# Kernel tuning notes

Measured on AMD Instinct MI355X. Metric: run time of the kernel, lower is better.

## Reference

```python
import jax, jax.numpy as jnp
import numpy as np
from jax import lax

V, D, H, HD, L, E, HID, TOPK, B, T = 32000, 1024, 16, 64, 2, 4, 2048, 2, 1, 1024
EPS = 1e-8


def setup_inputs() -> dict:
    key = jax.random.key(0)
    ks = jax.random.split(key, 10)
    s = 0.02
    so = 0.02 / np.sqrt(2 * L)  # o_proj / down_proj init std
    return dict(
        idx=jax.random.randint(ks[0], (B, T), 0, V),
        tok_emb=jax.random.normal(ks[1], (V, D), jnp.float32) * s,
        attn_norm_w=jnp.ones((L, D), jnp.float32),
        q_w=jax.random.normal(ks[2], (L, D, D), jnp.float32) * s,
        q_b=jnp.zeros((L, D), jnp.float32),
        kv_w=jax.random.normal(ks[3], (L, D, 2 * D), jnp.float32) * s,
        kv_b=jnp.zeros((L, 2 * D), jnp.float32),
        o_w=jax.random.normal(ks[4], (L, D, D), jnp.float32) * so,
        o_b=jnp.zeros((L, D), jnp.float32),
        ffn_norm_w=jnp.ones((L, D), jnp.float32),
        router_w=jax.random.normal(ks[5], (L, D, E), jnp.float32) * s,
        gate_w=jax.random.normal(ks[6], (L, E, D, HID), jnp.float32) * s,
        up_w=jax.random.normal(ks[7], (L, E, D, HID), jnp.float32) * s,
        down_w=jax.random.normal(ks[8], (L, E, HID, D), jnp.float32) * so,
        lnf_w=jnp.ones((D,), jnp.float32),
    )


def _rms(x, w):
    return x / jnp.sqrt(jnp.mean(x * x, axis=-1, keepdims=True) + EPS) * w


def reference(idx, tok_emb, attn_norm_w, q_w, q_b, kv_w, kv_b, o_w, o_b,
              ffn_norm_w, router_w, gate_w, up_w, down_w, lnf_w):
    x = tok_emb[idx]  # [B,T,D]

    # ALiBi bias and causal mask (built once; block_size == T here)
    slopes = jnp.arange(1, H + 1, dtype=jnp.float32) / H          # [H]
    pos = jnp.arange(T, dtype=jnp.float32)
    alibi = slopes[:, None, None] * (pos[None, None, :] - pos[None, :, None])  # [H,T,T]
    causal = jnp.arange(T)[None, :] > jnp.arange(T)[:, None]      # True above diagonal

    for l in range(L):
        # --- causal self-attention with ALiBi ---
        h = _rms(x, attn_norm_w[l])
        q = (h @ q_w[l] + q_b[l]).reshape(B, T, H, HD)
        kv = (h @ kv_w[l] + kv_b[l]).reshape(B, T, 2, H, HD)
        k, v = kv[:, :, 0], kv[:, :, 1]
        att = jnp.einsum('bqhd,bkhd->bhqk', q, k) * (1.0 / np.sqrt(HD))
        att = att + alibi[None]
        att = jnp.where(causal, -jnp.inf, att)
        a = jax.nn.softmax(att, axis=-1)
        y = jnp.einsum('bhqk,bkhd->bqhd', a, v).reshape(B, T, D)
        x = x + y @ o_w[l] + o_b[l]

        # --- MoE FFN (top-k routing, SwiGLU experts, depth-scaled down_proj) ---
        hm = _rms(x, ffn_norm_w[l]).reshape(B * T, D)             # [N,D]
        rlog = hm @ router_w[l]                                   # [N,E]
        vals, sel = lax.top_k(rlog, TOPK)                         # [N,K]
        w = jax.nn.softmax(vals.astype(jnp.float32), axis=-1).astype(hm.dtype)
        # dense per-expert compute, combined sparsely via routing weights
        g = jax.nn.silu(jnp.einsum('nd,edh->enh', hm, gate_w[l])) \
            * jnp.einsum('nd,edh->enh', hm, up_w[l])              # [E,N,HID]
        out_e = jnp.einsum('enh,ehd->end', g, down_w[l]) * (1.0 / np.sqrt(l + 1))
        combine = jnp.sum(jax.nn.one_hot(sel, E, dtype=hm.dtype) * w[..., None], axis=1)  # [N,E]
        moe = jnp.einsum('ne,end->nd', combine, out_e).reshape(B, T, D)
        x = x + moe

    logits = _rms(x, lnf_w) @ tok_emb.T  # tied head weight
    return logits
```

## Files before the change

kernel.cpp:

```cpp
#include <hip/hip_runtime.h>
#include <cmath>

typedef __attribute__((ext_vector_type(8))) _Float16 f16x8;
typedef __attribute__((ext_vector_type(8))) unsigned short u16x8;
typedef __attribute__((ext_vector_type(4))) float f32x4;

#define DEV static __device__ __forceinline__

constexpr int Dm   = 1024;
constexpr int HIDm = 2048;
constexpr int NT   = 1024;
constexpr int NV   = 32000;
constexpr float EPSf  = 1e-8f;
constexpr float LOSC  = 4096.0f;
constexpr float ILOSC = 1.0f / 4096.0f;

DEV unsigned short h2u(_Float16 h){ union{_Float16 h; unsigned short u;} v; v.h=h; return v.u; }

DEV f32x4 MF(f16x8 a, f16x8 b, f32x4 c){ return __builtin_amdgcn_mfma_f32_16x16x32_f16(a,b,c,0,0,0); }

typedef __attribute__((address_space(1))) void GV;
typedef __attribute__((address_space(3))) void LV;
DEV void gll16(const void* g, void* l){
  __builtin_amdgcn_global_load_lds((GV*)(__UINTPTR_TYPE__)g, (LV*)l, 16, 0, 0);
}

DEV int swk(int lane){ return (((lane&3) ^ ((lane>>3)&3))*8); }
DEV int rdc(int fr, int fg){ return ((fg ^ ((fr>>1)&3))*8); }

template<int SPLIT>
DEV void st_sp(unsigned short* __restrict__ hi, unsigned short* __restrict__ lo, size_t o, float v){
  _Float16 hh = (_Float16)v;
  hi[o] = h2u(hh);
  if constexpr (SPLIT==3) lo[o] = h2u((_Float16)((v - (float)hh)*LOSC));
}

__global__ __launch_bounds__(256) void k_init(
    const int* __restrict__ idx, const float* __restrict__ emb,
    float* __restrict__ x, unsigned short* __restrict__ emb16, int gbase)
{
  const int b = blockIdx.x;
  if (b < gbase){
    const size_t i = ((size_t)b*256 + threadIdx.x)*8;
    const float4 v0 = *(const float4*)&emb[i];
    const float4 v1 = *(const float4*)&emb[i+4];
    u16x8 h;
    h[0]=h2u((_Float16)v0.x); h[1]=h2u((_Float16)v0.y);
    h[2]=h2u((_Float16)v0.z); h[3]=h2u((_Float16)v0.w);
    h[4]=h2u((_Float16)v1.x); h[5]=h2u((_Float16)v1.y);
    h[6]=h2u((_Float16)v1.z); h[7]=h2u((_Float16)v1.w);
    *(u16x8*)&emb16[i] = h;
  } else {
    const int t = b - gbase;
    const int d = threadIdx.x*4;
    *(float4*)&x[(size_t)t*Dm + d] = *(const float4*)&emb[(size_t)idx[t]*Dm + d];
  }
}

template<int SPLIT>
__global__ __launch_bounds__(256) void k_rms(
    const float* __restrict__ x, const float* __restrict__ w,
    unsigned short* __restrict__ ohi, unsigned short* __restrict__ olo)
{
  const int t = blockIdx.x, tid = threadIdx.x;
  const float* row = x + (size_t)t*Dm;
  float s = 0.f;
  #pragma unroll
  for (int i=0;i<4;++i){ const float v = row[tid + i*256]; s += v*v; }
  #pragma unroll
  for (int d=1; d<64; d<<=1) s += __shfl_xor(s, d);
  __shared__ float red[4];
  if ((tid&63)==0) red[tid>>6] = s;
  __syncthreads();
  const float tot = red[0]+red[1]+red[2]+red[3];
  const float rstd = rsqrtf(tot*(1.0f/Dm) + EPSf);
  #pragma unroll
  for (int i=0;i<4;++i){
    const int c = tid + i*256;
    st_sp<SPLIT>(ohi, olo, (size_t)t*Dm + c, row[c]*rstd*w[c]);
  }
}

template<int SPLIT>
__global__ __launch_bounds__(256) void k_fuse_o(
    const float* __restrict__ part, const float* __restrict__ ob,
    const float* __restrict__ fnw, const float* __restrict__ rw,
    float* __restrict__ x, unsigned short* __restrict__ hhi,
    unsigned short* __restrict__ hlo, float* __restrict__ cmb)
{
  const int t = blockIdx.x, tid = threadIdx.x, wv = tid>>6, lane = tid&63;
  const int c = tid*4;
  float4 s = *(float4*)&x[(size_t)t*Dm + c];
  #pragma unroll
  for (int z=0; z<4; ++z){
    const float4 p = *(const float4*)&part[((size_t)z*NT + t)*Dm + c];
    s.x+=p.x; s.y+=p.y; s.z+=p.z; s.w+=p.w;
  }
  const float4 b4 = *(const float4*)&ob[c];
  s.x+=b4.x; s.y+=b4.y; s.z+=b4.z; s.w+=b4.w;
  *(float4*)&x[(size_t)t*Dm + c] = s;

  float ss = s.x*s.x + s.y*s.y + s.z*s.z + s.w*s.w;
  #pragma unroll
  for (int d=1; d<64; d<<=1) ss += __shfl_xor(ss, d);
  __shared__ float red[4];
  if (lane==0) red[wv] = ss;
  __syncthreads();
  const float rstd = rsqrtf((red[0]+red[1]+red[2]+red[3])*(1.0f/Dm) + EPSf);

  const float4 w4 = *(const float4*)&fnw[c];
  const float sv[4] = {s.x,s.y,s.z,s.w};
  const float wv4[4] = {w4.x,w4.y,w4.z,w4.w};
  float hm[4];
  float lg[4] = {0.f,0.f,0.f,0.f};
  #pragma unroll
  for (int j=0;j<4;++j){
    hm[j] = sv[j]*rstd*wv4[j];
    st_sp<SPLIT>(hhi, hlo, (size_t)t*Dm + c + j, hm[j]);
    const float4 r4 = *(const float4*)&rw[(size_t)(c+j)*4];
    lg[0] += hm[j]*r4.x; lg[1] += hm[j]*r4.y; lg[2] += hm[j]*r4.z; lg[3] += hm[j]*r4.w;
  }
  #pragma unroll
  for (int d=1; d<64; d<<=1){
    lg[0]+=__shfl_xor(lg[0],d); lg[1]+=__shfl_xor(lg[1],d);
    lg[2]+=__shfl_xor(lg[2],d); lg[3]+=__shfl_xor(lg[3],d);
  }
  __shared__ float red2[4][4];
  if (lane==0){ red2[wv][0]=lg[0]; red2[wv][1]=lg[1]; red2[wv][2]=lg[2]; red2[wv][3]=lg[3]; }
  __syncthreads();
  if (tid==0){
    float L[4];
    #pragma unroll
    for (int e=0;e<4;++e) L[e] = red2[0][e]+red2[1][e]+red2[2][e]+red2[3][e];
    int s0 = 0;
    for (int e=1;e<4;++e) if (L[e] > L[s0]) s0 = e;
    int s1 = -1;
    for (int e=0;e<4;++e){ if (e==s0) continue; if (s1<0 || L[e] > L[s1]) s1 = e; }
    const float eb2 = expf(L[s1] - L[s0]);
    const float inv = 1.0f/(1.0f + eb2);
    float o[4] = {0.f,0.f,0.f,0.f};
    o[s0] = inv; o[s1] = eb2*inv;
    cmb[t*4+0]=o[0]; cmb[t*4+1]=o[1]; cmb[t*4+2]=o[2]; cmb[t*4+3]=o[3];
  }
}

__global__ __launch_bounds__(256) void k_fuse_moe(
    const float* __restrict__ part, const float* __restrict__ cmb,
    const float* __restrict__ w, float* __restrict__ x,
    unsigned short* __restrict__ dst, int writex)
{
  const int t = blockIdx.x, tid = threadIdx.x, wv = tid>>6, lane = tid&63;
  const int c = tid*4;
  float4 s = *(float4*)&x[(size_t)t*Dm + c];
  #pragma unroll
  for (int e=0; e<4; ++e){
    if (cmb[(size_t)t*4 + e] > 0.f){
      const float4 p0 = *(const float4*)&part[((size_t)(e*2+0)*NT + t)*Dm + c];
      const float4 p1 = *(const float4*)&part[((size_t)(e*2+1)*NT + t)*Dm + c];
      s.x+=p0.x+p1.x; s.y+=p0.y+p1.y; s.z+=p0.z+p1.z; s.w+=p0.w+p1.w;
    }
  }
  if (writex) *(float4*)&x[(size_t)t*Dm + c] = s;
  float ss = s.x*s.x + s.y*s.y + s.z*s.z + s.w*s.w;
  #pragma unroll
  for (int d=1; d<64; d<<=1) ss += __shfl_xor(ss, d);
  __shared__ float red[4];
  if (lane==0) red[wv] = ss;
  __syncthreads();
  const float rstd = rsqrtf((red[0]+red[1]+red[2]+red[3])*(1.0f/Dm) + EPSf);
  const float4 w4 = *(const float4*)&w[c];
  const float sv[4] = {s.x,s.y,s.z,s.w};
  const float wv4[4] = {w4.x,w4.y,w4.z,w4.w};
  #pragma unroll
  for (int j=0;j<4;++j)
    dst[(size_t)t*Dm + c + j] = h2u((_Float16)(sv[j]*rstd*wv4[j]));
}

__global__ __launch_bounds__(256) void k_scan(
    const float* __restrict__ cmb, int* __restrict__ tl,
    float* __restrict__ cwl, int* __restrict__ cnt)
{
  const int e = threadIdx.x>>6, lane = threadIdx.x&63;
  int base = 0;
  for (int t0=0; t0<NT; t0+=64){
    const float w = cmb[(size_t)(t0+lane)*4 + e];
    const unsigned long long m = __ballot(w > 0.f);
    const int pre = __popcll(m & ((1ull<<lane)-1ull));
    if (w > 0.f){ tl[e*NT + base + pre] = t0+lane; cwl[e*NT + base + pre] = w; }
    base += __popcll(m);
  }
  if (lane==0) cnt[e] = base;
}

template<int SPLIT>
DEV void wconv_tile(const float* __restrict__ W, unsigned short* __restrict__ Whi,
                    unsigned short* __restrict__ Wlo, int K, int N, int n0, int k0,
                    float (*tile)[65], int t)
{
  const int r = t>>2;
  #pragma unroll
  for (int i=0;i<4;++i){
    const int c = (t&3)*16 + i*4;
    *(float4*)&tile[r][c] = *(const float4*)&W[(size_t)(k0+r)*N + n0 + c];
  }
  __syncthreads();
  const int n = t>>2;
  #pragma unroll
  for (int i=0;i<2;++i){
    const int kc = (t&3)*8 + i*32;
    u16x8 hi, lo;
    #pragma unroll
    for (int j=0;j<8;++j){
      const float v = tile[kc+j][n];
      const _Float16 hh = (_Float16)v;
      hi[j] = h2u(hh);
      if constexpr (SPLIT==3) lo[j] = h2u((_Float16)((v-(float)hh)*LOSC));
      else lo[j] = 0;
    }
    *(u16x8*)&Whi[(size_t)(n0+n)*K + k0 + kc] = hi;
    if constexpr (SPLIT==3) *(u16x8*)&Wlo[(size_t)(n0+n)*K + k0 + kc] = lo;
  }
}

template<int SPLIT>
__global__ __launch_bounds__(256) void k_wconv(
    const float* __restrict__ W, unsigned short* __restrict__ Whi,
    unsigned short* __restrict__ Wlo, int K, int N)
{
  __shared__ float tile[64][65];
  const size_t eb = (size_t)blockIdx.z * (size_t)K * N;
  wconv_tile<SPLIT>(W + eb, Whi + eb, Wlo + eb, K, N, blockIdx.x*64, blockIdx.y*64,
                    tile, threadIdx.x);
}

template<int SPLIT>
__global__ __launch_bounds__(256) void k_wconv_qkvo(
    const float* __restrict__ qw, const float* __restrict__ kvw, const float* __restrict__ ow,
    unsigned short* __restrict__ Wh, unsigned short* __restrict__ Wl,
    unsigned short* __restrict__ WOh, unsigned short* __restrict__ WOl)
{
  __shared__ float tile[64][65];
  const int b = blockIdx.x, t = threadIdx.x;
  if (b < 256){
    wconv_tile<SPLIT>(qw, Wh, Wl, Dm, Dm, (b&15)*64, (b>>4)*64, tile, t);
  } else if (b < 768){
    const int c = b - 256;
    wconv_tile<SPLIT>(kvw, Wh + (size_t)Dm*Dm, Wl + (size_t)Dm*Dm,
                      Dm, 2*Dm, (c&31)*64, (c>>5)*64, tile, t);
  } else {
    const int c = b - 768;
    wconv_tile<SPLIT>(ow, WOh, WOl, Dm, Dm, (c&15)*64, (c>>4)*64, tile, t);
  }
}

template<int SPLIT>
__global__ __launch_bounds__(256) void k_wconv_gu(
    const float* __restrict__ gw, const float* __restrict__ uw,
    unsigned short* __restrict__ WGh, unsigned short* __restrict__ WGl,
    unsigned short* __restrict__ WUh, unsigned short* __restrict__ WUl)
{
  __shared__ float tile[64][65];
  const int b = blockIdx.x, t = threadIdx.x;
  const int half = b >> 11;
  const int c = b & 2047;
  const int e = c >> 9, cc = c & 511;
  const size_t eb = (size_t)e * (size_t)Dm * HIDm;
  const int n0 = (cc&31)*64, k0 = (cc>>5)*64;
  if (half == 0)
    wconv_tile<SPLIT>(gw + eb, WGh + eb, WGl + eb, Dm, HIDm, n0, k0, tile, t);
  else
    wconv_tile<SPLIT>(uw + eb, WUh + eb, WUl + eb, Dm, HIDm, n0, k0, tile, t);
}

template<int SPLIT, int ZMODE>
__global__ __launch_bounds__(256) void k_mm(
    const unsigned short* __restrict__ Ahi, const unsigned short* __restrict__ Alo,
    const unsigned short* __restrict__ Bhi, const unsigned short* __restrict__ Blo,
    float* __restrict__ part, int lda, int ldb, int K, int ldo, int nx)
{
  constexpr int PL = (SPLIT==3)?2:1;
  __shared__ __align__(16) unsigned short As[PL][128][32];
  __shared__ __align__(16) unsigned short Bs[PL][128][32];
  const int xcd = blockIdx.x & 7, ii = blockIdx.x >> 3;
  const int w = xcd * (int)(gridDim.x >> 3) + ii;
  const int g = w >> 3, yy = w & 7;
  const int n0 = (g % nx)*128, r0 = yy*128, zz = g / nx;
  const int tid=threadIdx.x, wv=tid>>6, lane=tid&63, fr=lane&15, fg=lane>>4;
  const int wr=(wv>>1)*64, wc=(wv&1)*64;
  const int sr=lane>>2, sk=swk(lane);
  const int rc = rdc(fr, fg);

  const f32x4 z4={0.f,0.f,0.f,0.f};
  f32x4 accM[4][4], accC[4][4];
  #pragma unroll
  for (int i=0;i<4;++i)
    #pragma unroll
    for (int j=0;j<4;++j){ accM[i][j]=z4; accC[i][j]=z4; }

  for (int kt=0; kt<K; kt+=32){
    #pragma unroll
    for (int i=0;i<2;++i){
      const int rr = wv*32 + i*16 + sr;
      size_t ao, bo;
      if constexpr (ZMODE==2){
        ao = (size_t)(r0+rr)*lda + zz*K + kt + sk;
        bo = (size_t)(n0+rr)*ldb + zz*K + kt + sk;
      } else {
        ao = (size_t)(r0+rr)*lda + kt + sk;
        bo = (size_t)(n0+rr)*ldb + kt + sk;
      }
      gll16(&Ahi[ao], &As[0][wv*32+i*16][0]);
      if constexpr (SPLIT==3) gll16(&Alo[ao], &As[1][wv*32+i*16][0]);
      gll16(&Bhi[bo], &Bs[0][wv*32+i*16][0]);
      if constexpr (SPLIT==3) gll16(&Blo[bo], &Bs[1][wv*32+i*16][0]);
    }
    __syncthreads();
    f16x8 a[4][PL], b[4][PL];
    #pragma unroll
    for (int rt=0;rt<4;++rt)
      #pragma unroll
      for (int p=0;p<PL;++p) a[rt][p] = *(const f16x8*)&As[p][wr+rt*16+fr][rc];
    #pragma unroll
    for (int ct=0;ct<4;++ct)
      #pragma unroll
      for (int p=0;p<PL;++p) b[ct][p] = *(const f16x8*)&Bs[p][wc+ct*16+fr][rc];
    #pragma unroll
    for (int rt=0;rt<4;++rt)
      #pragma unroll
      for (int ct=0;ct<4;++ct){
        accM[rt][ct] = MF(a[rt][0], b[ct][0], accM[rt][ct]);
        if constexpr (SPLIT==3){
          accC[rt][ct] = MF(a[rt][0], b[ct][1], accC[rt][ct]);
          accC[rt][ct] = MF(a[rt][1], b[ct][0], accC[rt][ct]);
        }
      }
    __syncthreads();
  }

  #pragma unroll
  for (int rt=0;rt<4;++rt)
    #pragma unroll
    for (int ct=0;ct<4;++ct)
      #pragma unroll
      for (int j=0;j<4;++j){
        const int row = r0 + wr + rt*16 + fg*4 + j;
        const int col = n0 + wc + ct*16 + fr;
        float v = accM[rt][ct][j];
        if constexpr (SPLIT==3) v += accC[rt][ct][j]*ILOSC;
        part[((size_t)zz*NT + row)*ldo + col] = v;
      }
}

template<int SPLIT>
__global__ __launch_bounds__(256) void k_comb_qkvt(
    const float* __restrict__ part, const float* __restrict__ qb, const float* __restrict__ kvb,
    unsigned short* __restrict__ qhi, unsigned short* __restrict__ qlo,
    unsigned short* __restrict__ khi, unsigned short* __restrict__ klo,
    unsigned short* __restrict__ vthi, unsigned short* __restrict__ vtlo)
{
  __shared__ float tile[64][65];
  const int bid = blockIdx.x, tid = threadIdx.x;
  if (bid < 1024){
    const int t = bid;
    #pragma unroll
    for (int i=0;i<2;++i){
      const int col = tid*4 + i*1024;
      const float4 p0 = *(const float4*)&part[(size_t)t*3072 + col];
      const float4 p1 = *(const float4*)&part[((size_t)NT + t)*3072 + col];
      float v[4] = {p0.x+p1.x, p0.y+p1.y, p0.z+p1.z, p0.w+p1.w};
      #pragma unroll
      for (int j=0;j<4;++j){
        const int c = col + j;
        if (c < Dm) st_sp<SPLIT>(qhi, qlo, (size_t)t*Dm + c, v[j] + qb[c]);
        else        st_sp<SPLIT>(khi, klo, (size_t)t*Dm + (c-Dm), v[j] + kvb[c-Dm]);
      }
    }
  } else {
    const int c = bid - 1024;
    const int d0 = (c&15)*64, t0 = (c>>4)*64;
    {
      const int tl_ = tid>>2, dc = (tid&3)*16;
      #pragma unroll
      for (int i=0;i<4;++i){
        const int d = dc + i*4;
        const float4 p0 = *(const float4*)&part[(size_t)(t0+tl_)*3072 + 2048 + d0 + d];
        const float4 p1 = *(const float4*)&part[((size_t)NT + t0+tl_)*3072 + 2048 + d0 + d];
        tile[tl_][d+0] = p0.x+p1.x + kvb[1024+d0+d+0];
        tile[tl_][d+1] = p0.y+p1.y + kvb[1024+d0+d+1];
        tile[tl_][d+2] = p0.z+p1.z + kvb[1024+d0+d+2];
        tile[tl_][d+3] = p0.w+p1.w + kvb[1024+d0+d+3];
      }
    }
    __syncthreads();
    #pragma unroll
    for (int i=0;i<2;++i){
      const int u = tid + i*256;
      const int dl = u>>3, tch = (u&7)*8;
      u16x8 hi, lo;
      #pragma unroll
      for (int j=0;j<8;++j){
        const float v = tile[tch+j][dl];
        const _Float16 hh = (_Float16)v;
        hi[j] = h2u(hh);
        if constexpr (SPLIT==3) lo[j] = h2u((_Float16)((v-(float)hh)*LOSC));
        else lo[j] = 0;
      }
      *(u16x8*)&vthi[(size_t)(d0+dl)*NT + t0 + tch] = hi;
      if constexpr (SPLIT==3) *(u16x8*)&vtlo[(size_t)(d0+dl)*NT + t0 + tch] = lo;
    }
  }
}

template<int SPLIT>
__global__ __launch_bounds__(256) void k_down(
    const unsigned short* __restrict__ Ahi, const unsigned short* __restrict__ Alo,
    const unsigned short* __restrict__ Bhi, const unsigned short* __restrict__ Blo,
    const int* __restrict__ tl, const int* __restrict__ cnt,
    float* __restrict__ part)
{
  constexpr int PL = (SPLIT==3)?2:1;
  const int xcd = blockIdx.x & 7, ii = blockIdx.x >> 3;
  const int w = xcd*64 + ii;
  const int g = w >> 3, yy = w & 7;
  const int zz = g >> 3, e = zz >> 1, ks = zz & 1;
  const int r0 = yy*128, n0 = (g&7)*128;
  const int cn = cnt[e];
  if (r0 >= cn) return;
  __shared__ __align__(16) unsigned short As[PL][128][32];
  __shared__ __align__(16) unsigned short Bs[PL][128][32];
  __shared__ int tl_s[128];
  const int tid=threadIdx.x, wv=tid>>6, lane=tid&63, fr=lane&15, fg=lane>>4;
  const int wr=(wv>>1)*64, wc=(wv&1)*64;
  const int sr=lane>>2, sk=swk(lane);
  const int rc = rdc(fr, fg);
  if (tid < 128) tl_s[tid] = (r0+tid < cn) ? tl[e*NT + r0 + tid] : -1;

  const f32x4 z4={0.f,0.f,0.f,0.f};
  f32x4 accM[4][4], accC[4][4];
  #pragma unroll
  for (int i=0;i<4;++i)
    #pragma unroll
    for (int j=0;j<4;++j){ accM[i][j]=z4; accC[i][j]=z4; }

  const int kbeg = ks*1024, kend = kbeg + 1024;
  for (int kt=kbeg; kt<kend; kt+=32){
    #pragma unroll
    for (int i=0;i<2;++i){
      const int rr = wv*32 + i*16 + sr;
      const size_t ao = (size_t)((e<<10) + r0 + rr)*HIDm + kt + sk;
      const size_t bo = (size_t)e*((size_t)Dm*HIDm) + (size_t)(n0+rr)*HIDm + kt + sk;
      gll16(&Ahi[ao], &As[0][wv*32+i*16][0]);
      if constexpr (SPLIT==3) gll16(&Alo[ao], &As[1][wv*32+i*16][0]);
      gll16(&Bhi[bo], &Bs[0][wv*32+i*16][0]);
      if constexpr (SPLIT==3) gll16(&Blo[bo], &Bs[1][wv*32+i*16][0]);
    }
    __syncthreads();
    f16x8 a[4][PL], b[4][PL];
    #pragma unroll
    for (int rt=0;rt<4;++rt)
      #pragma unroll
      for (int p=0;p<PL;++p) a[rt][p] = *(const f16x8*)&As[p][wr+rt*16+fr][rc];
    #pragma unroll
    for (int ct=0;ct<4;++ct)
      #pragma unroll
      for (int p=0;p<PL;++p) b[ct][p] = *(const f16x8*)&Bs[p][wc+ct*16+fr][rc];
    #pragma unroll
    for (int rt=0;rt<4;++rt)
      #pragma unroll
      for (int ct=0;ct<4;++ct){
        accM[rt][ct] = MF(a[rt][0], b[ct][0], accM[rt][ct]);
        if constexpr (SPLIT==3){
          accC[rt][ct] = MF(a[rt][0], b[ct][1], accC[rt][ct]);
          accC[rt][ct] = MF(a[rt][1], b[ct][0], accC[rt][ct]);
        }
      }
    __syncthreads();
  }

  #pragma unroll
  for (int rt=0;rt<4;++rt)
    #pragma unroll
    for (int ct=0;ct<4;++ct)
      #pragma unroll
      for (int j=0;j<4;++j){
        const int i = wr + rt*16 + fg*4 + j;
        const int col = n0 + wc + ct*16 + fr;
        float v = accM[rt][ct][j];
        if constexpr (SPLIT==3) v += accC[rt][ct][j]*ILOSC;
        const int tok = tl_s[i];
        if (tok >= 0) part[((size_t)zz*NT + tok)*Dm + col] = v;
      }
}

template<int SPLIT>
__global__ __launch_bounds__(512) void k_guf(
    const unsigned short* __restrict__ Ahi, const unsigned short* __restrict__ Alo,
    const unsigned short* __restrict__ Ghi, const unsigned short* __restrict__ Glo,
    const unsigned short* __restrict__ Uhi, const unsigned short* __restrict__ Ulo,
    const int* __restrict__ tl, const float* __restrict__ cwl, const int* __restrict__ cnt,
    unsigned short* __restrict__ Hhi, unsigned short* __restrict__ Hlo, float scale)
{
  constexpr int PL=(SPLIT==3)?2:1;
  const int xcd = blockIdx.x & 7, ii = blockIdx.x >> 3;
  const int w = xcd*128 + ii;
  const int g = w >> 3, yy = w & 7;
  const int e = g >> 5, n0 = (g & 31)*64, r0 = yy*128;
  const int cn = cnt[e];
  if (r0 >= cn) return;
  __shared__ __align__(16) unsigned short As[PL][128][32];
  __shared__ __align__(16) unsigned short Gs[PL][64][32];
  __shared__ __align__(16) unsigned short Us[PL][64][32];
  __shared__ float cw_s[128];
  const int tid=threadIdx.x, wv=tid>>6, lane=tid&63, fr=lane&15, fg=lane>>4;
  const int wr=(wv>>1)*32, wc=(wv&1)*32;
  const int sr=lane>>2, sk=swk(lane);
  const int rc = rdc(fr, fg);
  const size_t ebW = (size_t)e * ((size_t)HIDm*Dm);
  if (tid < 128) cw_s[tid] = (r0+tid < cn) ? cwl[e*NT + r0 + tid]*scale : 0.f;

  const int lrA = r0 + wv*16 + sr;
  const int tokA = tl[e*NT + (lrA < cn ? lrA : cn-1)];
  const size_t abase = (size_t)tokA*Dm + sk;
  const int rrB = (wv&3)*16 + sr;
  const size_t bbase = ebW + (size_t)(n0+rrB)*Dm + sk;

  const f32x4 z4={0.f,0.f,0.f,0.f};
  f32x4 aGM[2][2],aGC[2][2],aUM[2][2],aUC[2][2];
  #pragma unroll
  for (int i=0;i<2;++i)
    #pragma unroll
    for (int j=0;j<2;++j){ aGM[i][j]=z4; aGC[i][j]=z4; aUM[i][j]=z4; aUC[i][j]=z4; }

  for (int kt=0; kt<Dm; kt+=32){
    gll16(&Ahi[abase + kt], &As[0][wv*16][0]);
    if constexpr (SPLIT==3) gll16(&Alo[abase + kt], &As[1][wv*16][0]);
    if (wv < 4){
      gll16(&Ghi[bbase + kt], &Gs[0][(wv&3)*16][0]);
      if constexpr (SPLIT==3) gll16(&Glo[bbase + kt], &Gs[1][(wv&3)*16][0]);
    } else {
      gll16(&Uhi[bbase + kt], &Us[0][(wv&3)*16][0]);
      if constexpr (SPLIT==3) gll16(&Ulo[bbase + kt], &Us[1][(wv&3)*16][0]);
    }
    __syncthreads();
    f16x8 a[2][PL], bg[2][PL], bu[2][PL];
    #pragma unroll
    for (int rt=0;rt<2;++rt)
      #pragma unroll
      for (int p=0;p<PL;++p) a[rt][p] = *(const f16x8*)&As[p][wr+rt*16+fr][rc];
    #pragma unroll
    for (int ct=0;ct<2;++ct)
      #pragma unroll
      for (int p=0;p<PL;++p){
        bg[ct][p] = *(const f16x8*)&Gs[p][wc+ct*16+fr][rc];
        bu[ct][p] = *(const f16x8*)&Us[p][wc+ct*16+fr][rc];
      }
    #pragma unroll
    for (int rt=0;rt<2;++rt)
      #pragma unroll
      for (int ct=0;ct<2;++ct){
        aGM[rt][ct] = MF(a[rt][0], bg[ct][0], aGM[rt][ct]);
        aUM[rt][ct] = MF(a[rt][0], bu[ct][0], aUM[rt][ct]);
        if constexpr (SPLIT==3){
          aGC[rt][ct] = MF(a[rt][0], bg[ct][1], aGC[rt][ct]);
          aGC[rt][ct] = MF(a[rt][1], bg[ct][0], aGC[rt][ct]);
          aUC[rt][ct] = MF(a[rt][0], bu[ct][1], aUC[rt][ct]);
          aUC[rt][ct] = MF(a[rt][1], bu[ct][0], aUC[rt][ct]);
        }
      }
    __syncthreads();
  }
  #pragma unroll
  for (int rt=0;rt<2;++rt)
    #pragma unroll
    for (int ct=0;ct<2;++ct)
      #pragma unroll
      for (int j=0;j<4;++j){
        const int i = wr + rt*16 + fg*4 + j;
        const int row = r0 + i;
        const int col = n0 + wc + ct*16 + fr;
        float g2 = aGM[rt][ct][j], u = aUM[rt][ct][j];
        if constexpr (SPLIT==3){ g2 += aGC[rt][ct][j]*ILOSC; u += aUC[rt][ct][j]*ILOSC; }
        const float cw = cw_s[i];
        const float h = (g2/(1.0f + expf(-g2))) * u * cw;
        st_sp<SPLIT>(Hhi, Hlo, (size_t)((e<<10) + row)*HIDm + col, h);
      }
}

__global__ __launch_bounds__(256) void k_lg(
    const unsigned short* __restrict__ Ahi, const float* __restrict__ emb,
    float* __restrict__ out)
{
  __shared__ __align__(16) unsigned short As[128][32];
  __shared__ __align__(16) unsigned short Bs[128][32];
  const int tid=threadIdx.x, wv=tid>>6, lane=tid&63, fr=lane&15, fg=lane>>4;
  const int w = (blockIdx.x & 7)*250 + (blockIdx.x >> 3);
  const int n0 = (w>>3)*128, r0 = (w&7)*128;
  const int wr=(wv>>1)*64, wc=(wv&1)*64;
  const int sr=lane>>2, sk=swk(lane);
  const int rc = rdc(fr, fg);
  const int br = tid>>1;
  const f32x4 z4={0.f,0.f,0.f,0.f};
  f32x4 acc[4][4];
  #pragma unroll
  for (int i=0;i<4;++i)
    #pragma unroll
    for (int j=0;j<4;++j) acc[i][j]=z4;

  for (int kt=0; kt<Dm; kt+=32){
    #pragma unroll
    for (int i=0;i<2;++i){
      const int rr = wv*32 + i*16 + sr;
      gll16(&Ahi[(size_t)(r0+rr)*Dm + kt + sk], &As[wv*32+i*16][0]);
    }
    {
      const int bc = (tid&1)*16;
      const float* s = &emb[(size_t)(n0+br)*Dm + kt + bc];
      const float4 v0 = *(const float4*)s;
      const float4 v1 = *(const float4*)(s+4);
      const float4 v2 = *(const float4*)(s+8);
      const float4 v3 = *(const float4*)(s+12);
      u16x8 h0, h1;
      h0[0]=h2u((_Float16)v0.x); h0[1]=h2u((_Float16)v0.y);
      h0[2]=h2u((_Float16)v0.z); h0[3]=h2u((_Float16)v0.w);
      h0[4]=h2u((_Float16)v1.x); h0[5]=h2u((_Float16)v1.y);
      h0[6]=h2u((_Float16)v1.z); h0[7]=h2u((_Float16)v1.w);
      h1[0]=h2u((_Float16)v2.x); h1[1]=h2u((_Float16)v2.y);
      h1[2]=h2u((_Float16)v2.z); h1[3]=h2u((_Float16)v2.w);
      h1[4]=h2u((_Float16)v3.x); h1[5]=h2u((_Float16)v3.y);
      h1[6]=h2u((_Float16)v3.z); h1[7]=h2u((_Float16)v3.w);
      const int s_ = (br>>1)&3;
      const int u0 = (tid&1)*2;
      *(u16x8*)&Bs[br][(u0^s_)*8]     = h0;
      *(u16x8*)&Bs[br][((u0+1)^s_)*8] = h1;
    }
    __syncthreads();
    f16x8 a[4], b[4];
    #pragma unroll
    for (int rt=0;rt<4;++rt) a[rt] = *(const f16x8*)&As[wr+rt*16+fr][rc];
    #pragma unroll
    for (int ct=0;ct<4;++ct) b[ct] = *(const f16x8*)&Bs[wc+ct*16+fr][rc];
    #pragma unroll
    for (int rt=0;rt<4;++rt)
      #pragma unroll
      for (int ct=0;ct<4;++ct) acc[rt][ct] = MF(a[rt], b[ct], acc[rt][ct]);
    __syncthreads();
  }
  #pragma unroll
  for (int rt=0;rt<4;++rt)
    #pragma unroll
    for (int ct=0;ct<4;++ct)
      #pragma unroll
      for (int j=0;j<4;++j)
        out[(size_t)(r0+wr+rt*16+fg*4+j)*NV + n0+wc+ct*16+fr] = acc[rt][ct][j];
}

__global__ __launch_bounds__(512) void k_lg16(
    const unsigned short* __restrict__ Ahi, const unsigned short* __restrict__ B16,
    float* __restrict__ out)
{
  __shared__ __align__(16) unsigned short As[256][64];
  __shared__ __align__(16) unsigned short Bs[256][64];
  const int tid=threadIdx.x, wv=tid>>6, lane=tid&63, fr=lane&15, fg=lane>>4;
  const int xcd = blockIdx.x & 7, ii = blockIdx.x >> 3;
  const int w = (xcd < 4 ? xcd*63 : 252 + (xcd-4)*62) + ii;
  const int n0 = (w>>2)*256, r0 = (w&3)*256;
  const int wrow=(wv>>2)*128, wcol=(wv&3)*64;
  const int srow = lane>>3;
  const int sk = (((lane&7) ^ srow)*8);
  const f32x4 z4={0.f,0.f,0.f,0.f};
  f32x4 acc[8][4];
  #pragma unroll
  for (int i=0;i<8;++i)
    #pragma unroll
    for (int j=0;j<4;++j) acc[i][j]=z4;

  for (int kt=0; kt<Dm; kt+=64){
    #pragma unroll
    for (int i=0;i<4;++i){
      const int rr = wv*32 + i*8 + srow;
      gll16(&Ahi[(size_t)(r0+rr)*Dm + kt + sk], &As[wv*32+i*8][0]);
      gll16(&B16[(size_t)(n0+rr)*Dm + kt + sk], &Bs[wv*32+i*8][0]);
    }
    __syncthreads();
    #pragma unroll
    for (int kk=0;kk<2;++kk){
      f16x8 a[8], b[4];
      #pragma unroll
      for (int rt=0;rt<8;++rt)
        a[rt] = *(const f16x8*)&As[wrow+rt*16+fr][(((kk*4+fg) ^ (fr&7))*8)];
      #pragma unroll
      for (int ct=0;ct<4;++ct)
        b[ct] = *(const f16x8*)&Bs[wcol+ct*16+fr][(((kk*4+fg) ^ (fr&7))*8)];
      #pragma unroll
      for (int rt=0;rt<8;++rt)
        #pragma unroll
        for (int ct=0;ct<4;++ct) acc[rt][ct] = MF(a[rt], b[ct], acc[rt][ct]);
    }
    __syncthreads();
  }
  #pragma unroll
  for (int rt=0;rt<8;++rt)
    #pragma unroll
    for (int ct=0;ct<4;++ct)
      #pragma unroll
      for (int j=0;j<4;++j)
        out[(size_t)(r0+wrow+rt*16+fg*4+j)*NV + n0+wcol+ct*16+fr] = acc[rt][ct][j];
}

template<int SPLIT>
__global__ __launch_bounds__(256) void k_attn(
    const unsigned short* __restrict__ qhi, const unsigned short* __restrict__ qlo,
    const unsigned short* __restrict__ khi, const unsigned short* __restrict__ klo,
    const unsigned short* __restrict__ vthi, const unsigned short* __restrict__ vtlo,
    unsigned short* __restrict__ yhi, unsigned short* __restrict__ ylo)
{
  constexpr int PL = (SPLIT==3) ? 2 : 1;
  const int qt = blockIdx.x, hd = blockIdx.y;
  const int tid = threadIdx.x, wv = tid>>6, lane = tid&63;
  const int fr = lane&15, fg = lane>>4;
  const int rbase = qt*64 + wv*16;
  const float slope = (float)(hd+1) * (1.0f/16.0f);

  __shared__ __align__(16) unsigned short Ps[4][PL][16][32];

  f16x8 aq[2][PL];
  #pragma unroll
  for (int c=0;c<2;++c){
    const size_t off = (size_t)(rbase+fr)*Dm + hd*64 + c*32 + fg*8;
    aq[c][0] = *(const f16x8*)&qhi[off];
    if constexpr (SPLIT==3) aq[c][1] = *(const f16x8*)&qlo[off];
  }

  const f32x4 z4 = {0.f,0.f,0.f,0.f};
  f32x4 yM[4], yC[4];
  #pragma unroll
  for (int ct=0;ct<4;++ct){ yM[ct]=z4; yC[ct]=z4; }
  float m[4], lsum[4];
  #pragma unroll
  for (int j=0;j<4;++j){ m[j] = -INFINITY; lsum[j] = 0.f; }

  const int nkt = qt*2 + 2;
  for (int kt=0; kt<nkt; ++kt){
    f32x4 sM[2], sC[2];
    sM[0]=z4; sM[1]=z4; sC[0]=z4; sC[1]=z4;
    #pragma unroll
    for (int kh=0; kh<2; ++kh){
      #pragma unroll
      for (int c=0;c<2;++c){
        const size_t off = (size_t)(kt*32 + kh*16 + fr)*Dm + hd*64 + c*32 + fg*8;
        const f16x8 b0 = *(const f16x8*)&khi[off];
        sM[kh] = MF(aq[c][0], b0, sM[kh]);
        if constexpr (SPLIT==3){
          const f16x8 b1 = *(const f16x8*)&klo[off];
          sC[kh] = MF(aq[c][0], b1, sC[kh]);
          sC[kh] = MF(aq[c][1], b0, sC[kh]);
        }
      }
    }
    float sv[2][4], mx[4];
    #pragma unroll
    for (int j=0;j<4;++j) mx[j] = -INFINITY;
    #pragma unroll
    for (int kh=0; kh<2; ++kh)
      #pragma unroll
      for (int j=0;j<4;++j){
        const int kcol = kt*32 + kh*16 + fr;
        const int row  = rbase + fg*4 + j;
        float s = sM[kh][j];
        if constexpr (SPLIT==3) s += sC[kh][j]*ILOSC;
        s = s*0.125f + slope*(float)(kcol - row);
        sv[kh][j] = (kcol > row) ? -INFINITY : s;
        mx[j] = fmaxf(mx[j], sv[kh][j]);
      }
    #pragma unroll
    for (int d=1; d<16; d<<=1)
      #pragma unroll
      for (int j=0;j<4;++j) mx[j] = fmaxf(mx[j], __shfl_xor(mx[j], d));
    float resc[4];
    #pragma unroll
    for (int j=0;j<4;++j){
      const float mn = fmaxf(m[j], mx[j]);
      resc[j] = expf(m[j] - mn);
      m[j] = mn;
    }
    float p[2][4], psum[4];
    #pragma unroll
    for (int j=0;j<4;++j) psum[j] = 0.f;
    #pragma unroll
    for (int kh=0;kh<2;++kh)
      #pragma unroll
      for (int j=0;j<4;++j){
        const float pv = (sv[kh][j] == -INFINITY) ? 0.f : expf(sv[kh][j] - m[j]);
        p[kh][j] = pv; psum[j] += pv;
      }
    #pragma unroll
    for (int d=1; d<16; d<<=1)
      #pragma unroll
      for (int j=0;j<4;++j) psum[j] += __shfl_xor(psum[j], d);
    #pragma unroll
    for (int j=0;j<4;++j) lsum[j] = lsum[j]*resc[j] + psum[j];
    #pragma unroll
    for (int ct=0;ct<4;++ct)
      #pragma unroll
      for (int j=0;j<4;++j){ yM[ct][j]*=resc[j]; yC[ct][j]*=resc[j]; }
    #pragma unroll
    for (int kh=0;kh<2;++kh)
      #pragma unroll
      for (int j=0;j<4;++j){
        const float pv = p[kh][j];
        _Float16 ph = (_Float16)pv;
        Ps[wv][0][fg*4+j][kh*16+fr] = h2u(ph);
        if constexpr (SPLIT==3)
          Ps[wv][1][fg*4+j][kh*16+fr] = h2u((_Float16)((pv-(float)ph)*LOSC));
      }
    asm volatile("s_waitcnt lgkmcnt(0)" ::: "memory");
    f16x8 pa[PL];
    pa[0] = *(const f16x8*)&Ps[wv][0][fr][fg*8];
    if constexpr (SPLIT==3) pa[1] = *(const f16x8*)&Ps[wv][1][fr][fg*8];
    #pragma unroll
    for (int ct=0;ct<4;++ct){
      const size_t off = (size_t)(hd*64 + ct*16 + fr)*NT + kt*32 + fg*8;
      const f16x8 v0 = *(const f16x8*)&vthi[off];
      yM[ct] = MF(pa[0], v0, yM[ct]);
      if constexpr (SPLIT==3){
        const f16x8 v1 = *(const f16x8*)&vtlo[off];
        yC[ct] = MF(pa[0], v1, yC[ct]);
        yC[ct] = MF(pa[1], v0, yC[ct]);
      }
    }
    asm volatile("s_waitcnt lgkmcnt(0)" ::: "memory");
  }
  #pragma unroll
  for (int ct=0;ct<4;++ct)
    #pragma unroll
    for (int j=0;j<4;++j){
      float v = yM[ct][j];
      if constexpr (SPLIT==3) v += yC[ct][j]*ILOSC;
      v /= lsum[j];
      const size_t off = (size_t)(rbase + fg*4 + j)*Dm + hd*64 + ct*16 + fr;
      st_sp<SPLIT>(yhi, ylo, off, v);
    }
}

struct Ptrs {
  float* x; float* cmb; float* part; float* cwl; int* tl; int* cnt;
  unsigned short *hhi,*hlo,*qhi,*qlo,*khi,*klo,*vthi,*vtlo,*yhi,*ylo,*Hhi,*Hlo;
  unsigned short *Wqkvh,*Wqkvl,*WOh,*WOl,*WGh,*WGl,*WUh,*WUl,*WDh,*WDl;
};

template<int S>
static void run_layer(const Ptrs& P, int l,
    const float* anw, const float* qw, const float* qb, const float* kvw, const float* kvb,
    const float* ow, const float* ob, const float* fnw, const float* rw,
    const float* gw, const float* uw, const float* dw,
    const float* nextw, unsigned short* nextdst, int writex, float scale, hipStream_t stream)
{
  (void)anw;
  k_wconv_qkvo<S><<<dim3(1024), dim3(256), 0, stream>>>(
      qw + (size_t)l*Dm*Dm, kvw + (size_t)l*Dm*2*Dm, ow + (size_t)l*Dm*Dm,
      P.Wqkvh, P.Wqkvl, P.WOh, P.WOl);
  k_mm<S,2><<<dim3(384), dim3(256), 0, stream>>>(P.hhi, P.hlo, P.Wqkvh, P.Wqkvl,
      P.part, Dm, Dm, 512, 3072, 24);
  k_comb_qkvt<S><<<dim3(1280), dim3(256), 0, stream>>>(P.part, qb + l*Dm, kvb + l*2*Dm,
      P.qhi, P.qlo, P.khi, P.klo, P.vthi, P.vtlo);
  k_attn<S><<<dim3(16,16), dim3(256), 0, stream>>>(P.qhi,P.qlo,P.khi,P.klo,P.vthi,P.vtlo,P.yhi,P.ylo);
  k_mm<S,2><<<dim3(256), dim3(256), 0, stream>>>(P.yhi, P.ylo, P.WOh, P.WOl,
      P.part, Dm, Dm, 256, Dm, 8);
  k_fuse_o<S><<<dim3(NT), dim3(256), 0, stream>>>(P.part, ob + l*Dm, fnw + l*Dm,
      rw + (size_t)l*Dm*4, P.x, P.hhi, P.hlo, P.cmb);
  k_scan<<<dim3(1), dim3(256), 0, stream>>>(P.cmb, P.tl, P.cwl, P.cnt);
  k_wconv_gu<S><<<dim3(4096), dim3(256), 0, stream>>>(
      gw + (size_t)l*4*Dm*HIDm, uw + (size_t)l*4*Dm*HIDm, P.WGh, P.WGl, P.WUh, P.WUl);
  k_guf<S><<<dim3(1024), dim3(512), 0, stream>>>(P.hhi, P.hlo, P.WGh, P.WGl, P.WUh, P.WUl,
      P.tl, P.cwl, P.cnt, P.Hhi, P.Hlo, scale);
  k_wconv<S><<<dim3(16,32,4), dim3(256), 0, stream>>>(dw + (size_t)l*4*HIDm*Dm, P.WDh, P.WDl, HIDm, Dm);
  k_down<S><<<dim3(512), dim3(256), 0, stream>>>(P.Hhi, P.Hlo, P.WDh, P.WDl,
      P.tl, P.cnt, P.part);
  k_fuse_moe<<<dim3(NT), dim3(256), 0, stream>>>(P.part, P.cmb, nextw, P.x, nextdst, writex);
}

extern "C" void kernel_launch(void* const* d_in, const int* in_sizes, int n_in,
                              void* d_out, int out_size, void* d_ws, size_t ws_size,
                              hipStream_t stream)
{
  (void)in_sizes; (void)n_in; (void)out_size;
  const int*   idx = (const int*)d_in[0];
  const float* emb = (const float*)d_in[1];
  const float* anw = (const float*)d_in[2];
  const float* qw  = (const float*)d_in[3];
  const float* qb  = (const float*)d_in[4];
  const float* kvw = (const float*)d_in[5];
  const float* kvb = (const float*)d_in[6];
  const float* ow  = (const float*)d_in[7];
  const float* ob  = (const float*)d_in[8];
  const float* fnw = (const float*)d_in[9];
  const float* rw  = (const float*)d_in[10];
  const float* gw  = (const float*)d_in[11];
  const float* uw  = (const float*)d_in[12];
  const float* dw  = (const float*)d_in[13];
  const float* lnf = (const float*)d_in[14];

  constexpr size_t MB = (size_t)1<<20;
  constexpr size_t KB = (size_t)1<<10;
  char* sc = (char*)d_out;
  Ptrs P;
  P.x     = (float*)sc;
  P.hhi   = (unsigned short*)(sc + 4*MB);
  P.hlo   = (unsigned short*)(sc + 6*MB);
  P.qhi   = (unsigned short*)(sc + 8*MB);
  P.qlo   = (unsigned short*)(sc + 10*MB);
  P.khi   = (unsigned short*)(sc + 12*MB);
  P.klo   = (unsigned short*)(sc + 14*MB);
  P.vthi  = (unsigned short*)(sc + 16*MB);
  P.vtlo  = (unsigned short*)(sc + 18*MB);
  P.yhi   = (unsigned short*)(sc + 20*MB);
  P.ylo   = (unsigned short*)(sc + 22*MB);
  P.cmb   = (float*)(sc + 24*MB);
  P.tl    = (int*)(sc + 24*MB + 64*KB);
  P.cwl   = (float*)(sc + 24*MB + 128*KB);
  P.cnt   = (int*)(sc + 24*MB + 192*KB);
  P.Hhi   = (unsigned short*)(sc + 25*MB);
  P.Hlo   = (unsigned short*)(sc + 41*MB);
  P.Wqkvh = (unsigned short*)(sc + 57*MB);
  P.Wqkvl = (unsigned short*)(sc + 63*MB);
  P.WOh   = (unsigned short*)(sc + 69*MB);
  P.WOl   = (unsigned short*)(sc + 71*MB);
  P.WGh   = (unsigned short*)(sc + 57*MB);
  P.WGl   = (unsigned short*)(sc + 73*MB);
  P.WUh   = (unsigned short*)(sc + 89*MB);
  P.WUl   = (unsigned short*)(sc + 105*MB);
  P.WDh   = (unsigned short*)(sc + 57*MB);
  P.WDl   = (unsigned short*)(sc + 73*MB);
  P.part  = (float*)(sc + 89*MB);
  unsigned short* xhat  = (unsigned short*)d_ws;
  unsigned short* emb16 = (unsigned short*)((char*)d_ws + 2*MB);
  const bool big_ws = ws_size >= 68*MB;
  float* out = (float*)d_out;

  const int gbase = big_ws ? 16000 : 0;
  k_init<<<dim3(gbase + NT), dim3(256), 0, stream>>>(idx, emb, P.x, emb16, gbase);
  k_rms<3><<<dim3(NT), dim3(256), 0, stream>>>(P.x, anw, P.hhi, P.hlo);

  run_layer<3>(P, 0, anw, qw, qb, kvw, kvb, ow, ob, fnw, rw, gw, uw, dw,
               anw + Dm, P.hhi, 1, 1.0f, stream);
  run_layer<1>(P, 1, anw, qw, qb, kvw, kvb, ow, ob, fnw, rw, gw, uw, dw,
               lnf, xhat, 0, 0.70710678f, stream);

  if (big_ws)
    k_lg16<<<dim3(500), dim3(512), 0, stream>>>(xhat, emb16, out);
  else
    k_lg<<<dim3(2000), dim3(256), 0, stream>>>(xhat, emb, out);
}
```

Baseline: 812.8 us.

## Drop XCD-aware block swizzle and split attention into single-wave blocks

The GEMM, gate-up and down kernels stop remapping linear block IDs to spread neighbouring tiles across XCDs and use plain 3D grid indices instead. The attention kernel goes from 4-wave blocks covering 64 query rows to single-wave blocks covering 16 rows, giving more, smaller blocks with finer causal load balancing. This loses the intended L2 locality of the swizzle and drops K/V sharing across waves within a block, in exchange for simpler indexing and better scheduling granularity.

```diff
diff --git a/kernel.cpp b/kernel.cpp
--- a/kernel.cpp
+++ b/kernel.cpp
@@ -276,16 +276,13 @@
 __global__ __launch_bounds__(256) void k_mm(
     const unsigned short* __restrict__ Ahi, const unsigned short* __restrict__ Alo,
     const unsigned short* __restrict__ Bhi, const unsigned short* __restrict__ Blo,
-    float* __restrict__ part, int lda, int ldb, int K, int ldo, int nx)
+    float* __restrict__ part, int lda, int ldb, int K, int ldo)
 {
   constexpr int PL = (SPLIT==3)?2:1;
   __shared__ __align__(16) unsigned short As[PL][128][32];
   __shared__ __align__(16) unsigned short Bs[PL][128][32];
-  const int xcd = blockIdx.x & 7, ii = blockIdx.x >> 3;
-  const int w = xcd * (int)(gridDim.x >> 3) + ii;
-  const int g = w >> 3, yy = w & 7;
-  const int n0 = (g % nx)*128, r0 = yy*128, zz = g / nx;
   const int tid=threadIdx.x, wv=tid>>6, lane=tid&63, fr=lane&15, fg=lane>>4;
+  const int n0=blockIdx.x*128, r0=blockIdx.y*128, zz=blockIdx.z;
   const int wr=(wv>>1)*64, wc=(wv&1)*64;
   const int sr=lane>>2, sk=swk(lane);
   const int rc = rdc(fr, fg);
@@ -419,11 +416,8 @@
     float* __restrict__ part)
 {
   constexpr int PL = (SPLIT==3)?2:1;
-  const int xcd = blockIdx.x & 7, ii = blockIdx.x >> 3;
-  const int w = xcd*64 + ii;
-  const int g = w >> 3, yy = w & 7;
-  const int zz = g >> 3, e = zz >> 1, ks = zz & 1;
-  const int r0 = yy*128, n0 = (g&7)*128;
+  const int zz = blockIdx.z, e = zz>>1, ks = zz&1;
+  const int r0 = blockIdx.y*128, n0 = blockIdx.x*128;
   const int cn = cnt[e];
   if (r0 >= cn) return;
   __shared__ __align__(16) unsigned short As[PL][128][32];
@@ -501,10 +495,7 @@
     unsigned short* __restrict__ Hhi, unsigned short* __restrict__ Hlo, float scale)
 {
   constexpr int PL=(SPLIT==3)?2:1;
-  const int xcd = blockIdx.x & 7, ii = blockIdx.x >> 3;
-  const int w = xcd*128 + ii;
-  const int g = w >> 3, yy = w & 7;
-  const int e = g >> 5, n0 = (g & 31)*64, r0 = yy*128;
+  const int e = blockIdx.z, r0 = blockIdx.y*128, n0 = blockIdx.x*64;
   const int cn = cnt[e];
   if (r0 >= cn) return;
   __shared__ __align__(16) unsigned short As[PL][128][32];
@@ -708,7 +699,7 @@
 }
 
 template<int SPLIT>
-__global__ __launch_bounds__(256) void k_attn(
+__global__ __launch_bounds__(64) void k_attn(
     const unsigned short* __restrict__ qhi, const unsigned short* __restrict__ qlo,
     const unsigned short* __restrict__ khi, const unsigned short* __restrict__ klo,
     const unsigned short* __restrict__ vthi, const unsigned short* __restrict__ vtlo,
@@ -716,12 +707,12 @@
 {
   constexpr int PL = (SPLIT==3) ? 2 : 1;
   const int qt = blockIdx.x, hd = blockIdx.y;
-  const int tid = threadIdx.x, wv = tid>>6, lane = tid&63;
+  const int lane = threadIdx.x;
   const int fr = lane&15, fg = lane>>4;
-  const int rbase = qt*64 + wv*16;
+  const int rbase = qt*16;
   const float slope = (float)(hd+1) * (1.0f/16.0f);
 
-  __shared__ __align__(16) unsigned short Ps[4][PL][16][32];
+  __shared__ __align__(16) unsigned short Ps[PL][16][32];
 
   f16x8 aq[2][PL];
   #pragma unroll
@@ -739,7 +730,7 @@
   #pragma unroll
   for (int j=0;j<4;++j){ m[j] = -INFINITY; lsum[j] = 0.f; }
 
-  const int nkt = qt*2 + 2;
+  const int nkt = qt/2 + 1;
   for (int kt=0; kt<nkt; ++kt){
     f32x4 sM[2], sC[2];
     sM[0]=z4; sM[1]=z4; sC[0]=z4; sC[1]=z4;
@@ -809,14 +800,14 @@
       for (int j=0;j<4;++j){
         const float pv = p[kh][j];
         _Float16 ph = (_Float16)pv;
-        Ps[wv][0][fg*4+j][kh*16+fr] = h2u(ph);
+        Ps[0][fg*4+j][kh*16+fr] = h2u(ph);
         if constexpr (SPLIT==3)
-          Ps[wv][1][fg*4+j][kh*16+fr] = h2u((_Float16)((pv-(float)ph)*LOSC));
+          Ps[1][fg*4+j][kh*16+fr] = h2u((_Float16)((pv-(float)ph)*LOSC));
       }
     asm volatile("s_waitcnt lgkmcnt(0)" ::: "memory");
     f16x8 pa[PL];
-    pa[0] = *(const f16x8*)&Ps[wv][0][fr][fg*8];
-    if constexpr (SPLIT==3) pa[1] = *(const f16x8*)&Ps[wv][1][fr][fg*8];
+    pa[0] = *(const f16x8*)&Ps[0][fr][fg*8];
+    if constexpr (SPLIT==3) pa[1] = *(const f16x8*)&Ps[1][fr][fg*8];
     #pragma unroll
     for (int ct=0;ct<4;++ct){
       const size_t off = (size_t)(hd*64 + ct*16 + fr)*NT + kt*32 + fg*8;
@@ -859,22 +850,22 @@
   k_wconv_qkvo<S><<<dim3(1024), dim3(256), 0, stream>>>(
       qw + (size_t)l*Dm*Dm, kvw + (size_t)l*Dm*2*Dm, ow + (size_t)l*Dm*Dm,
       P.Wqkvh, P.Wqkvl, P.WOh, P.WOl);
-  k_mm<S,2><<<dim3(384), dim3(256), 0, stream>>>(P.hhi, P.hlo, P.Wqkvh, P.Wqkvl,
-      P.part, Dm, Dm, 512, 3072, 24);
+  k_mm<S,2><<<dim3(24,8,2), dim3(256), 0, stream>>>(P.hhi, P.hlo, P.Wqkvh, P.Wqkvl,
+      P.part, Dm, Dm, 512, 3072);
   k_comb_qkvt<S><<<dim3(1280), dim3(256), 0, stream>>>(P.part, qb + l*Dm, kvb + l*2*Dm,
       P.qhi, P.qlo, P.khi, P.klo, P.vthi, P.vtlo);
-  k_attn<S><<<dim3(16,16), dim3(256), 0, stream>>>(P.qhi,P.qlo,P.khi,P.klo,P.vthi,P.vtlo,P.yhi,P.ylo);
-  k_mm<S,2><<<dim3(256), dim3(256), 0, stream>>>(P.yhi, P.ylo, P.WOh, P.WOl,
-      P.part, Dm, Dm, 256, Dm, 8);
+  k_attn<S><<<dim3(64,16), dim3(64), 0, stream>>>(P.qhi,P.qlo,P.khi,P.klo,P.vthi,P.vtlo,P.yhi,P.ylo);
+  k_mm<S,2><<<dim3(8,8,4), dim3(256), 0, stream>>>(P.yhi, P.ylo, P.WOh, P.WOl,
+      P.part, Dm, Dm, 256, Dm);
   k_fuse_o<S><<<dim3(NT), dim3(256), 0, stream>>>(P.part, ob + l*Dm, fnw + l*Dm,
       rw + (size_t)l*Dm*4, P.x, P.hhi, P.hlo, P.cmb);
   k_scan<<<dim3(1), dim3(256), 0, stream>>>(P.cmb, P.tl, P.cwl, P.cnt);
   k_wconv_gu<S><<<dim3(4096), dim3(256), 0, stream>>>(
       gw + (size_t)l*4*Dm*HIDm, uw + (size_t)l*4*Dm*HIDm, P.WGh, P.WGl, P.WUh, P.WUl);
-  k_guf<S><<<dim3(1024), dim3(512), 0, stream>>>(P.hhi, P.hlo, P.WGh, P.WGl, P.WUh, P.WUl,
+  k_guf<S><<<dim3(32,8,4), dim3(512), 0, stream>>>(P.hhi, P.hlo, P.WGh, P.WGl, P.WUh, P.WUl,
       P.tl, P.cwl, P.cnt, P.Hhi, P.Hlo, scale);
   k_wconv<S><<<dim3(16,32,4), dim3(256), 0, stream>>>(dw + (size_t)l*4*HIDm*Dm, P.WDh, P.WDl, HIDm, Dm);
-  k_down<S><<<dim3(512), dim3(256), 0, stream>>>(P.Hhi, P.Hlo, P.WDh, P.WDl,
+  k_down<S><<<dim3(8,8,8), dim3(256), 0, stream>>>(P.Hhi, P.Hlo, P.WDh, P.WDl,
       P.tl, P.cnt, P.part);
   k_fuse_moe<<<dim3(NT), dim3(256), 0, stream>>>(P.part, P.cmb, nextw, P.x, nextdst, writex);
 }
```

Measured after the change: 785.7 us. 1.03x faster.
